# Kernel tuning notes

Measured on AMD Instinct MI355X. Metric: run time of the kernel, lower is better.

The kernel has to match this reference:

```python
import jax, jax.numpy as jnp
import numpy as np

NUM_HEADS = 8
NUM_LAYERS = 6
NUM_POINTS = 25
# TrajParamIndex: X=0,Y=1,Z=2,VX=3,VY=4,AX=5,AY=6,YAW=7,LENGTH=8,WIDTH=9,HEIGHT=10


def _unit_cube_points(n=NUM_POINTS):
    m = int(np.sqrt(n))
    lin = np.linspace(-1.0, 1.0, m)
    pts = []
    for dim in range(3):
        for sign in (-1.0, 1.0):
            a, b = np.meshgrid(lin, lin, indexing='ij')
            s = np.full_like(a, sign)
            if dim == 0:
                p = np.stack([s, a, b], -1)
            elif dim == 1:
                p = np.stack([a, s, b], -1)
            else:
                p = np.stack([a, b, s], -1)
            pts.append(p.reshape(-1, 3))
    return jnp.asarray(np.concatenate(pts, 0), jnp.float32)  # [150,3]


def _ln(x, g, b):
    m = x.mean(-1, keepdims=True)
    v = ((x - m) ** 2).mean(-1, keepdims=True)
    return (x - m) / jnp.sqrt(v + 1e-5) * g + b


def _mha(q, k, v, wi, bi, wo, bo):
    E = q.shape[-1]
    d = E // NUM_HEADS
    qq = q @ wi[:E].T + bi[:E]
    kk = k @ wi[E:2 * E].T + bi[E:2 * E]
    vv = v @ wi[2 * E:].T + bi[2 * E:]
    B, S, _ = qq.shape
    Sk = kk.shape[1]
    qh = qq.reshape(B, S, NUM_HEADS, d)
    kh = kk.reshape(B, Sk, NUM_HEADS, d)
    vh = vv.reshape(B, Sk, NUM_HEADS, d)
    att = jnp.einsum('bqhd,bkhd->bhqk', qh, kh) / jnp.sqrt(jnp.float32(d))
    att = jax.nn.softmax(att, axis=-1)
    o = jnp.einsum('bhqk,bkhd->bqhd', att, vh).reshape(B, S, E)
    return o @ wo.T + bo


def _bilinear(feat, uv, valid):
    # feat [B,C,H,W], uv [B,M,2] in [0,1] (u along W), valid [B,M] -> [B,M,C]
    B, C, H, W = feat.shape
    px = uv[..., 0] * (W - 1)
    py = uv[..., 1] * (H - 1)
    x0 = jnp.floor(px)
    y0 = jnp.floor(py)
    wx = px - x0
    wy = py - y0
    x0i = jnp.clip(x0, 0, W - 1).astype(jnp.int32)
    x1i = jnp.clip(x0 + 1, 0, W - 1).astype(jnp.int32)
    y0i = jnp.clip(y0, 0, H - 1).astype(jnp.int32)
    y1i = jnp.clip(y0 + 1, 0, H - 1).astype(jnp.int32)
    flat = feat.reshape(B, C, H * W)
    take = jax.vmap(lambda f, i: f[:, i])  # [C,HW],[M] -> [C,M]
    f00 = take(flat, y0i * W + x0i)
    f01 = take(flat, y0i * W + x1i)
    f10 = take(flat, y1i * W + x0i)
    f11 = take(flat, y1i * W + x1i)
    wxb = wx[:, None, :]
    wyb = wy[:, None, :]
    out = (f00 * (1 - wxb) * (1 - wyb) + f01 * wxb * (1 - wyb)
           + f10 * (1 - wxb) * wyb + f11 * wxb * wyb)
    out = out * valid[:, None, :].astype(out.dtype)
    return out.transpose(0, 2, 1)


def _transform_points(box_pts, tp, ego_t, dt):
    # box_pts [B,N,P,3] local, tp [B,N,11], ego_t [B,4] (x,y,yaw,ts), dt [B]
    yaw = tp[..., 7][..., None]  # [B,N,1]
    c, s = jnp.cos(yaw), jnp.sin(yaw)
    lx, ly, lz = box_pts[..., 0], box_pts[..., 1], box_pts[..., 2]
    rx = lx * c - ly * s
    ry = lx * s + ly * c
    dtb = dt[:, None]  # [B,1]
    cx = tp[..., 0] + tp[..., 3] * dtb + 0.5 * tp[..., 5] * dtb ** 2  # [B,N]
    cy = tp[..., 1] + tp[..., 4] * dtb + 0.5 * tp[..., 6] * dtb ** 2
    cz = tp[..., 2]
    wx = rx + cx[..., None]
    wy = ry + cy[..., None]
    wz = lz + cz[..., None]
    ex = ego_t[:, 0][:, None, None]
    ey = ego_t[:, 1][:, None, None]
    eyaw = ego_t[:, 2][:, None, None]
    pxr = wx - ex
    pyr = wy - ey
    gx = pxr * jnp.cos(eyaw) + pyr * jnp.sin(eyaw)
    gy = -pxr * jnp.sin(eyaw) + pyr * jnp.cos(eyaw)
    return jnp.stack([gx, gy, wz], -1)


def _project(wp, cal):
    # wp [B,N,P,3], cal [B,8] = fx,fy,cx,cy,tx,ty,tz,cam_yaw -> uv in [0,1], valid
    fx, fy, cx0, cy0, tx, ty, tz, cyaw = [cal[:, i][:, None, None] for i in range(8)]
    px = wp[..., 0] - tx
    py = wp[..., 1] - ty
    pz = wp[..., 2] - tz
    fwd = px * jnp.cos(cyaw) + py * jnp.sin(cyaw)
    left = -px * jnp.sin(cyaw) + py * jnp.cos(cyaw)
    zc = fwd
    xc = -left
    yc = -pz
    vz = zc > 0.1
    zs = jnp.maximum(zc, 0.1)
    u = fx * xc / zs + cx0
    v = fy * yc / zs + cy0
    valid = vz & (u >= 0) & (u < 1) & (v >= 0) & (v < 1)
    return jnp.stack([u, v], -1), valid


def _forward(features, calib, ego_states, queries, query_pos,
             traj_w1, traj_b1, traj_w2, traj_b2,
             fm_w1, fm_b1, fm_w2, fm_b2,
             sa_in_w, sa_in_b, sa_out_w, sa_out_b,
             ca_in_w, ca_in_b, ca_out_w, ca_out_b,
             l1_w, l1_b, l2_w, l2_b,
             n1_g, n1_b, n2_g, n2_b, n3_g, n3_b):
    unit = _unit_cube_points()  # [P,3]
    P = unit.shape[0]
    cams, B, T = features.shape[0], features.shape[1], features.shape[2]
    Cf = features.shape[3]
    N = queries.shape[0]

    def traj_head(x):
        return jax.nn.relu(x @ traj_w1.T + traj_b1) @ traj_w2.T + traj_b2

    def feature_mlp(x):
        return jax.nn.relu(x @ fm_w1.T + fm_b1) @ fm_w2.T + fm_b2

    q = jnp.broadcast_to(queries[None], (B, N, queries.shape[1]))
    outputs = []
    for li in range(NUM_LAYERS):
        tp = traj_head(q)  # [B,N,11]
        outputs.append(tp)
        dims = tp[..., 8:11][:, :, None, :]  # [B,N,1,3] (L,W,H)
        box_pts = unit[None, None] * dims  # [B,N,P,3]
        acc = jnp.zeros((B, N, Cf), jnp.float32)
        for t in range(T):
            dt = ego_states[:, t, 3] - ego_states[:, -1, 3]  # [B]
            wp = _transform_points(box_pts, tp, ego_states[:, t], dt)
            for ci in range(cams):
                uv, valid = _project(wp, calib[ci])
                samp = _bilinear(features[ci, :, t], uv.reshape(B, N * P, 2),
                                 valid.reshape(B, N * P))  # [B,N*P,Cf]
                acc = acc + samp.reshape(B, N, P, Cf).sum(axis=2)
        agg = acc / jnp.float32(P * T * cams)
        mem = feature_mlp(agg)  # [B,N,Cf]
        # refine layer li (called without query_pos in decoder forward)
        sa = _mha(q, q, q, sa_in_w[li], sa_in_b[li], sa_out_w[li], sa_out_b[li])
        q = _ln(q + sa, n1_g[li], n1_b[li])
        ca = _mha(q, mem, mem, ca_in_w[li], ca_in_b[li], ca_out_w[li], ca_out_b[li])
        q = _ln(q + ca, n2_g[li], n2_b[li])
        ff = jax.nn.relu(q @ l1_w[li].T + l1_b[li]) @ l2_w[li].T + l2_b[li]
        q = _ln(q + ff, n3_g[li], n3_b[li])
    outputs.append(traj_head(q))
    return jnp.stack(outputs)  # [L+1,B,N,11]


def setup_inputs() -> dict:
    key = jax.random.key(0)
    ks = jax.random.split(key, 32)
    cams, B, T, Cf, H, W = 6, 1, 2, 256, 64, 160
    N, E, Dff, L = 128, 256, 512, NUM_LAYERS

    def rn(k, shape, scale=0.05):
        return jax.random.normal(k, shape, jnp.float32) * scale

    features = jax.random.normal(ks[0], (cams, B, T, Cf, H, W), jnp.float32)
    # calibration: fx,fy,cx,cy,tx,ty,tz,cam_yaw; cameras 8m behind origin along view dir
    cal = np.zeros((cams, B, 8), np.float32)
    for ci in range(cams):
        cyaw = ci * (2 * np.pi / cams)
        cal[ci, :, 0] = 1.2
        cal[ci, :, 1] = 1.6
        cal[ci, :, 2] = 0.5
        cal[ci, :, 3] = 0.5
        cal[ci, :, 4] = -8.0 * np.cos(cyaw)
        cal[ci, :, 5] = -8.0 * np.sin(cyaw)
        cal[ci, :, 6] = -0.5
        cal[ci, :, 7] = cyaw
    calib = jnp.asarray(cal)
    ego = np.zeros((B, T, 4), np.float32)
    for t in range(T):
        ego[:, t, 0] = 0.5 * t
        ego[:, t, 2] = 0.01 * t
        ego[:, t, 3] = 0.1 * t
    ego_states = jnp.asarray(ego)
    return {
        'features': features, 'calib': calib, 'ego_states': ego_states,
        'queries': rn(ks[1], (N, E), 1.0), 'query_pos': rn(ks[2], (N, E), 1.0),
        'traj_w1': rn(ks[3], (Dff, E)), 'traj_b1': jnp.zeros((Dff,), jnp.float32),
        'traj_w2': rn(ks[4], (11, Dff)), 'traj_b2': jnp.zeros((11,), jnp.float32),
        'fm_w1': rn(ks[5], (Dff, E)), 'fm_b1': jnp.zeros((Dff,), jnp.float32),
        'fm_w2': rn(ks[6], (E, Dff)), 'fm_b2': jnp.zeros((E,), jnp.float32),
        'sa_in_w': rn(ks[7], (L, 3 * E, E)), 'sa_in_b': jnp.zeros((L, 3 * E), jnp.float32),
        'sa_out_w': rn(ks[8], (L, E, E)), 'sa_out_b': jnp.zeros((L, E), jnp.float32),
        'ca_in_w': rn(ks[9], (L, 3 * E, E)), 'ca_in_b': jnp.zeros((L, 3 * E), jnp.float32),
        'ca_out_w': rn(ks[10], (L, E, E)), 'ca_out_b': jnp.zeros((L, E), jnp.float32),
        'l1_w': rn(ks[11], (L, Dff, E)), 'l1_b': jnp.zeros((L, Dff), jnp.float32),
        'l2_w': rn(ks[12], (L, E, Dff)), 'l2_b': jnp.zeros((L, E), jnp.float32),
        'n1_g': jnp.ones((L, E), jnp.float32), 'n1_b': jnp.zeros((L, E), jnp.float32),
        'n2_g': jnp.ones((L, E), jnp.float32), 'n2_b': jnp.zeros((L, E), jnp.float32),
        'n3_g': jnp.ones((L, E), jnp.float32), 'n3_b': jnp.zeros((L, E), jnp.float32),
    }


def reference(features, calib, ego_states, queries, query_pos,
              traj_w1, traj_b1, traj_w2, traj_b2,
              fm_w1, fm_b1, fm_w2, fm_b2,
              sa_in_w, sa_in_b, sa_out_w, sa_out_b,
              ca_in_w, ca_in_b, ca_out_w, ca_out_b,
              l1_w, l1_b, l2_w, l2_b,
              n1_g, n1_b, n2_g, n2_b, n3_g, n3_b):
    return _forward(features, calib, ego_states, queries, query_pos,
                    traj_w1, traj_b1, traj_w2, traj_b2,
                    fm_w1, fm_b1, fm_w2, fm_b2,
                    sa_in_w, sa_in_b, sa_out_w, sa_out_b,
                    ca_in_w, ca_in_b, ca_out_w, ca_out_b,
                    l1_w, l1_b, l2_w, l2_b,
                    n1_g, n1_b, n2_g, n2_b, n3_g, n3_b)
```

## Files before the change

### kernel.cpp

```cpp
#include <hip/hip_runtime.h>
#include <stdint.h>

typedef unsigned short u16;

#define DEV static __device__ __forceinline__

DEV float b2f(u16 u){ return __uint_as_float(((uint32_t)u) << 16); }
DEV u16 f2b(float f){ uint32_t x = __float_as_uint(f); return (u16)((x + 0x7fffu + ((x >> 16) & 1u)) >> 16); }
DEV int imin(int a, int b){ return a < b ? a : b; }
DEV int imax(int a, int b){ return a > b ? a : b; }

DEV int is_f32(const void* cal){
  float a = ((const float*)cal)[0];
  return (fabsf(a - 1.2f) < 1e-2f) ? 1 : 0;
}

DEV float ld(const void* p, size_t i, int f32){
  return f32 ? ((const float*)p)[i] : b2f(((const u16*)p)[i]);
}

__device__ float4 g_sawT[6*256*768/4];
__device__ float4 g_sowT[6*256*256/4];
__device__ float4 g_cawT[6*256*768/4];
__device__ float4 g_cowT[6*256*256/4];
__device__ float4 g_l1wT[6*256*512/4];
__device__ float4 g_l2wT[6*512*256/4];
__device__ float4 g_tw1T[256*512/4];
__device__ float4 g_fw1T[256*512/4];
__device__ float4 g_fw2T[512*256/4];

DEV float dotP(const float* x, const float4* wP, int col, const int N, const int K){
  const float4* p = wP + col;
  const float4* x4 = (const float4*)x;
  float s0=0.f,s1=0.f,s2=0.f,s3=0.f;
  #pragma unroll 8
  for(int k4 = 0; k4 < K/4; k4++){
    float4 w = p[(size_t)k4*N];
    float4 xv = x4[k4];
    s0 += xv.x*w.x; s1 += xv.y*w.y; s2 += xv.z*w.z; s3 += xv.w*w.w;
  }
  return (s0+s1)+(s2+s3);
}

DEV void dot2P(const float* x, const float4* wP, int c0, int c1, const int N,
               float* r0, float* r1){
  const float4* p0 = wP + c0;
  const float4* p1 = wP + c1;
  const float4* x4 = (const float4*)x;
  float a0=0,a1=0,a2=0,a3=0,b0=0,b1=0,b2=0,b3=0;
  #pragma unroll 8
  for(int k4 = 0; k4 < 64; k4++){
    float4 xv = x4[k4];
    float4 w0 = p0[(size_t)k4*N];
    float4 w1 = p1[(size_t)k4*N];
    a0+=xv.x*w0.x; a1+=xv.y*w0.y; a2+=xv.z*w0.z; a3+=xv.w*w0.w;
    b0+=xv.x*w1.x; b1+=xv.y*w1.y; b2+=xv.z*w1.z; b3+=xv.w*w1.w;
  }
  *r0=(a0+a1)+(a2+a3); *r1=(b0+b1)+(b2+b3);
}

DEV void dot3P(const float* x, const float4* wP, int t, float* r0, float* r1, float* r2){
  const float4* p0 = wP + t;
  const float4* p1 = wP + t + 256;
  const float4* p2 = wP + t + 512;
  const float4* x4 = (const float4*)x;
  float a0=0,a1=0,a2=0,a3=0,b0=0,b1=0,b2=0,b3=0,c0=0,c1=0,c2=0,c3=0;
  #pragma unroll 4
  for(int k4 = 0; k4 < 64; k4++){
    float4 xv = x4[k4];
    float4 w0 = p0[(size_t)k4*768];
    float4 w1 = p1[(size_t)k4*768];
    float4 w2 = p2[(size_t)k4*768];
    a0+=xv.x*w0.x; a1+=xv.y*w0.y; a2+=xv.z*w0.z; a3+=xv.w*w0.w;
    b0+=xv.x*w1.x; b1+=xv.y*w1.y; b2+=xv.z*w1.z; b3+=xv.w*w1.w;
    c0+=xv.x*w2.x; c1+=xv.y*w2.y; c2+=xv.z*w2.z; c3+=xv.w*w2.w;
  }
  *r0=(a0+a1)+(a2+a3); *r1=(b0+b1)+(b2+b3); *r2=(c0+c1)+(c2+c3);
}

DEV void kv_store_k(float* kT, int t, int qi, float val){
  int hh = t >> 5, i = t & 31;
  kT[((size_t)(hh*1024 + (i>>2)*128 + qi))*4 + (i&3)] = val;
}
DEV void kv_store_v(float* vP, int t, int qi, float val){
  vP[((size_t)((qi>>2)*256 + t))*4 + (qi&3)] = val;
}

DEV float attn_score(const float* qv, const float* kT, int hh, int k){
  const float4* kp = (const float4*)kT + hh*1024 + k;
  const float4* xq = (const float4*)(qv + hh*32);
  float s0=0.f, s1=0.f;
  #pragma unroll
  for(int i4 = 0; i4 < 8; i4 += 2){
    float4 w0 = kp[i4*128], w1 = kp[(i4+1)*128];
    float4 x0 = xq[i4],     x1 = xq[i4+1];
    s0 += x0.x*w0.x + x0.y*w0.y + x0.z*w0.z + x0.w*w0.w;
    s1 += x1.x*w1.x + x1.y*w1.y + x1.z*w1.z + x1.w*w1.w;
  }
  return s0+s1;
}

DEV float attn_av(const float* s, const float* vP, int hh, int t){
  const float4* vp = (const float4*)vP + t;
  const float4* sp = (const float4*)(s + hh*128);
  float a0=0.f, a1=0.f;
  #pragma unroll 8
  for(int k4 = 0; k4 < 32; k4 += 2){
    float4 w0 = vp[(size_t)k4*256], w1 = vp[(size_t)(k4+1)*256];
    float4 s0 = sp[k4],             s1 = sp[k4+1];
    a0 += s0.x*w0.x + s0.y*w0.y + s0.z*w0.z + s0.w*w0.w;
    a1 += s1.x*w1.x + s1.y*w1.y + s1.z*w1.z + s1.w*w1.w;
  }
  return a0+a1;
}

DEV float bsum256(float v, float* buf){
  int t = threadIdx.x;
  for(int off = 32; off > 0; off >>= 1) v += __shfl_xor(v, off);
  if((t & 63) == 0) buf[t >> 6] = v;
  __syncthreads();
  float r = buf[0] + buf[1] + buf[2] + buf[3];
  __syncthreads();
  return r;
}

DEV float lnorm(float r, const void* g, const void* b, size_t off, float* buf, int f32){
  float m = bsum256(r, buf) * (1.f/256.f);
  float d = r - m;
  float v = bsum256(d*d, buf) * (1.f/256.f);
  return d * rsqrtf(v + 1e-5f) * ld(g, off + threadIdx.x, f32) + ld(b, off + threadIdx.x, f32);
}

DEV void traj_headT(const float* qn, const void* b1, const void* w2, const void* b2,
                    float* hbuf, float* tp, void* out, int slot, int qi, int f32){
  int t = threadIdx.x;
  float h0, h1;
  dot2P(qn, g_tw1T, t, t + 256, 512, &h0, &h1);
  hbuf[t]     = fmaxf(0.f, ld(b1, t, f32)     + h0);
  hbuf[t+256] = fmaxf(0.f, ld(b1, t+256, f32) + h1);
  __syncthreads();
  if(t < 176){
    int o = t >> 4, lane = t & 15;
    float s = 0.f;
    for(int k = lane; k < 512; k += 16) s += hbuf[k] * ld(w2, o*512 + k, f32);
    for(int off = 8; off > 0; off >>= 1) s += __shfl_down(s, off, 16);
    if(lane == 0){
      s += ld(b2, o, f32);
      tp[qi*11 + o] = s;
      int oi = (slot*128 + qi)*11 + o;
      if(f32) ((float*)out)[oi] = s; else ((u16*)out)[oi] = f2b(s);
    }
  }
  __syncthreads();
}

DEV void softmax8(float* s){
  int t = threadIdx.x;
  int hh = t >> 5, lane = t & 31;
  float m = -1e30f;
  for(int k = lane; k < 128; k += 32) m = fmaxf(m, s[hh*128 + k]);
  for(int off = 16; off > 0; off >>= 1) m = fmaxf(m, __shfl_xor(m, off, 32));
  float ss = 0.f;
  for(int k = lane; k < 128; k += 32){
    float e = __expf(s[hh*128 + k] - m);
    s[hh*128 + k] = e; ss += e;
  }
  for(int off = 16; off > 0; off >>= 1) ss += __shfl_xor(ss, off, 32);
  float inv = 1.f / ss;
  for(int k = lane; k < 128; k += 32) s[hh*128 + k] *= inv;
}

__global__ __launch_bounds__(256) void k_wt(
    const void* saw, const void* sow, const void* caw, const void* cow,
    const void* l1w, const void* l2w, const void* tw1, const void* fw1, const void* fw2,
    const void* cal){
  int f32 = is_f32(cal);
  int t = threadIdx.x;
  __shared__ __align__(16) float tile[64*65];
  int bid = blockIdx.x;
  const void* src; float* dst; int N, K, NB, KB;
  if(bid < 288)      { src = saw; dst = (float*)g_sawT; N=768; K=256; NB=12; KB=4; }
  else if(bid < 384) { src = sow; dst = (float*)g_sowT; N=256; K=256; NB=4;  KB=4; bid -= 288; }
  else if(bid < 672) { src = caw; dst = (float*)g_cawT; N=768; K=256; NB=12; KB=4; bid -= 384; }
  else if(bid < 768) { src = cow; dst = (float*)g_cowT; N=256; K=256; NB=4;  KB=4; bid -= 672; }
  else if(bid < 960) { src = l1w; dst = (float*)g_l1wT; N=512; K=256; NB=8;  KB=4; bid -= 768; }
  else if(bid < 1152){ src = l2w; dst = (float*)g_l2wT; N=256; K=512; NB=4;  KB=8; bid -= 960; }
  else if(bid < 1184){ src = tw1; dst = (float*)g_tw1T; N=512; K=256; NB=8;  KB=4; bid -= 1152; }
  else if(bid < 1216){ src = fw1; dst = (float*)g_fw1T; N=512; K=256; NB=8;  KB=4; bid -= 1184; }
  else               { src = fw2; dst = (float*)g_fw2T; N=256; K=512; NB=4;  KB=8; bid -= 1216; }
  int nb = bid % NB;
  int kb = (bid / NB) % KB;
  int l  = bid / (NB*KB);
  for(int it = 0; it < 16; it++){
    int n = it*4 + (t >> 6);
    int k = t & 63;
    tile[n*65 + k] = ld(src, ((size_t)l*N + nb*64 + n)*K + kb*64 + k, f32);
  }
  __syncthreads();
  int kl = t & 3, nn = (t >> 2) & 15, wv = t >> 6;
  int n_local = wv*16 + nn;
  for(int k4 = 0; k4 < 16; k4++){
    int kcol = k4*4 + kl;
    size_t addr = (size_t)l*K*N + (((size_t)(kb*16 + k4))*N + nb*64 + n_local)*4 + kl;
    dst[addr] = tile[n_local*65 + kcol];
  }
}

__global__ __launch_bounds__(256) void k_trinit(const void* feat, u16* FTb, int use_ft,
    const void* queries, const void* tb1, const void* tw2, const void* tb2,
    const void* sab, const void* cal,
    float* q, float* tp, float* qrow, float* kTsa, float* vsa, float* acc, void* out){
  int f32 = is_f32(cal);
  int t = threadIdx.x;
  __shared__ __align__(16) uint32_t smem[64*65];
  if(blockIdx.x < 128){
    float* qn   = (float*)smem;
    float* hbuf = (float*)smem + 256;
    int qi = blockIdx.x;
    float v = ld(queries, qi*256 + t, f32);
    qn[t] = v; q[qi*256 + t] = v;
    __syncthreads();
    traj_headT(qn, tb1, tw2, tb2, hbuf, tp, out, 0, qi, f32);
    float c0, c1, c2;
    dot3P(qn, g_sawT, t, &c0, &c1, &c2);
    qrow[qi*256 + t] = ld(sab, t, f32)       + c0;
    kv_store_k(kTsa, t, qi, ld(sab, t + 256, f32) + c1);
    kv_store_v(vsa,  t, qi, ld(sab, t + 512, f32) + c2);
    acc[qi*256 + t] = 0.f;
    return;
  }
  if(!use_ft) return;
  int orig = blockIdx.x - 128;
  int swz  = (orig & 7) * 960 + (orig >> 3);
  int pch = swz % 160; int g = swz / 160;
  int cc = g & 3; int e = g >> 2;
  size_t rowbase = (size_t)(e*256 + cc*64);
  size_t poff = (size_t)pch*64;
  if(f32){
    #pragma unroll
    for(int pass = 0; pass < 4; pass++){
      int ch = pass*16 + (t >> 4);
      int pos = (t & 15)*4;
      const float* sp = (const float*)feat + (rowbase + ch)*10240 + poff + pos;
      float4 v = *(const float4*)sp;
      smem[(pos+0)*65 + ch] = f2b(v.x);
      smem[(pos+1)*65 + ch] = f2b(v.y);
      smem[(pos+2)*65 + ch] = f2b(v.z);
      smem[(pos+3)*65 + ch] = f2b(v.w);
    }
  } else {
    #pragma unroll
    for(int pass = 0; pass < 4; pass++){
      int ch = pass*16 + (t >> 4);
      int pos = (t & 15)*4;
      const u16* sp = (const u16*)feat + (rowbase + ch)*10240 + poff + pos;
      ushort4 v = *(const ushort4*)sp;
      smem[(pos+0)*65 + ch] = v.x;
      smem[(pos+1)*65 + ch] = v.y;
      smem[(pos+2)*65 + ch] = v.z;
      smem[(pos+3)*65 + ch] = v.w;
    }
  }
  __syncthreads();
  #pragma unroll
  for(int pass = 0; pass < 4; pass++){
    int pos = pass*16 + (t >> 4);
    int ch = (t & 15)*4;
    ushort4 v;
    v.x = (u16)smem[pos*65 + ch];
    v.y = (u16)smem[pos*65 + ch+1];
    v.z = (u16)smem[pos*65 + ch+2];
    v.w = (u16)smem[pos*65 + ch+3];
    *(ushort4*)&FTb[((size_t)(e*10240) + poff + pos)*256 + cc*64 + ch] = v;
  }
}

__global__ __launch_bounds__(256, 2) void k_samsa(const u16* FTb, const void* feat, int use_ft,
    const void* cal, const void* ego, const float* tp, float* acc,
    const float* q, const float* qrow, const float* kTsa, const float* vsa,
    const void* sob, const void* n1g, const void* n1b, const void* cab,
    int li, float* qs, float* qq){
  int t = threadIdx.x;
  int f32 = is_f32(cal);
  __shared__ __align__(16) float xa[256];
  __shared__ __align__(16) float s[1024];
  __shared__ __align__(16) float h[512];
  __shared__ float buf[8];
  __shared__ float tps[11];
  __shared__ int4  soff[152];
  __shared__ float4 sw[152];
  __shared__ float spx[152], spy[152];
  __shared__ int sval[152];
  __shared__ int plist[152];
  __shared__ int pcnt;

  if(blockIdx.x < 128){
    int qi = blockIdx.x;
    xa[t] = qrow[qi*256 + t];
    __syncthreads();
    for(int rep = 0; rep < 4; rep++){
      int idx = t + rep*256; int hh = idx >> 7, k = idx & 127;
      s[idx] = attn_score(xa, kTsa, hh, k) * 0.1767766952966369f;
    }
    __syncthreads();
    softmax8(s);
    __syncthreads();
    h[t] = attn_av(s, vsa, t >> 5, t);
    __syncthreads();
    float pr = ld(sob, (size_t)li*256 + t, f32) + dotP(h, g_sowT + (size_t)li*16384, t, 256, 256);
    float r = q[qi*256 + t] + pr;
    float y = lnorm(r, n1g, n1b, (size_t)li*256, buf, f32);
    qs[qi*256 + t] = y;
    __syncthreads();
    xa[t] = y;
    __syncthreads();
    qq[qi*256 + t] = ld(cab, (size_t)li*768 + t, f32)
                   + dotP(xa, g_cawT + (size_t)li*49152, t, 768, 256);
    return;
  }

  int sb = blockIdx.x - 128;
  int ob = (sb & 7) * 192 + (sb >> 3);
  int qi = ob & 127, e = ob >> 7;
  int ci = e >> 1, tt = e & 1;
  if(t == 0) pcnt = 0;
  if(t < 11) tps[t] = tp[qi*11 + t];
  __syncthreads();
  if(t < 150){
    float dt = ld(ego, tt*4 + 3, f32) - ld(ego, 7, f32);
    int face = t/25, rr = t%25, ii = rr/5, jj = rr%5;
    float av = -1.f + 0.5f*ii, bv = -1.f + 0.5f*jj;
    float sg = (face & 1) ? 1.f : -1.f; int dim = face >> 1;
    float ux = (dim == 0) ? sg : av;
    float uy = (dim == 0) ? av : ((dim == 1) ? sg : bv);
    float uz = (dim == 2) ? sg : bv;
    float lx = ux*tps[8], ly = uy*tps[9], lz = uz*tps[10];
    float yaw = tps[7];
    float cyw = cosf(yaw), syw = sinf(yaw);
    float rx = lx*cyw - ly*syw, ry = lx*syw + ly*cyw;
    float dt2 = 0.5f*dt*dt;
    float cxx = tps[0] + tps[3]*dt + tps[5]*dt2;
    float cyy = tps[1] + tps[4]*dt + tps[6]*dt2;
    float wx = rx + cxx, wy = ry + cyy, wz = lz + tps[2];
    float ex = ld(ego, tt*4, f32), ey = ld(ego, tt*4 + 1, f32), eyaw = ld(ego, tt*4 + 2, f32);
    float ce = cosf(eyaw), se = sinf(eyaw);
    float pxr = wx - ex, pyr = wy - ey;
    float gx = pxr*ce + pyr*se, gy = -pxr*se + pyr*ce;
    float fx = ld(cal, ci*8, f32),   fy = ld(cal, ci*8+1, f32);
    float cx0 = ld(cal, ci*8+2, f32), cy0 = ld(cal, ci*8+3, f32);
    float tx = ld(cal, ci*8+4, f32), ty = ld(cal, ci*8+5, f32);
    float tz = ld(cal, ci*8+6, f32), cw = ld(cal, ci*8+7, f32);
    float cc = cosf(cw), sc = sinf(cw);
    float pxc = gx - tx, pyc = gy - ty, pzc = wz - tz;
    float zc = pxc*cc + pyc*sc;
    float left = -pxc*sc + pyc*cc;
    float xc = -left, yc = -pzc;
    float zs = fmaxf(zc, 0.1f);
    float u = fx*xc/zs + cx0, vv = fy*yc/zs + cy0;
    bool val = (zc > 0.1f) && (u >= 0.f) && (u < 1.f) && (vv >= 0.f) && (vv < 1.f);
    float px = u*159.f, py = vv*63.f;
    spx[t] = px; spy[t] = py;
    float x0f = floorf(px), y0f = floorf(py);
    float wxf = px - x0f, wyf = py - y0f;
    int x0 = imin(imax((int)x0f, 0), 159), y0 = imin(imax((int)y0f, 0), 63);
    int x1 = imin(x0 + 1, 159), y1 = imin(y0 + 1, 63);
    soff[t] = make_int4((y0*160 + x0)*256, (y0*160 + x1)*256,
                        (y1*160 + x0)*256, (y1*160 + x1)*256);
    sw[t] = make_float4((1.f-wxf)*(1.f-wyf), wxf*(1.f-wyf), (1.f-wxf)*wyf, wxf*wyf);
    sval[t] = val ? 1 : 0;
    if(val){ int ix = atomicAdd(&pcnt, 1); plist[ix] = t; }
  }
  __syncthreads();
  float a = 0.f;
  if(use_ft){
    const u16* base = FTb + (size_t)e*10240*256 + t;
    int np = pcnt;
    int pp = 0;
    for(; pp + 4 <= np; pp += 4){
      int p0 = plist[pp], p1 = plist[pp+1], p2 = plist[pp+2], p3 = plist[pp+3];
      int4 o0 = soff[p0]; int4 o1 = soff[p1]; int4 o2 = soff[p2]; int4 o3 = soff[p3];
      float4 w0 = sw[p0]; float4 w1 = sw[p1]; float4 w2 = sw[p2]; float4 w3 = sw[p3];
      float v00 = b2f(base[o0.x]), v01 = b2f(base[o0.y]), v02 = b2f(base[o0.z]), v03 = b2f(base[o0.w]);
      float v10 = b2f(base[o1.x]), v11 = b2f(base[o1.y]), v12 = b2f(base[o1.z]), v13 = b2f(base[o1.w]);
      float v20 = b2f(base[o2.x]), v21 = b2f(base[o2.y]), v22 = b2f(base[o2.z]), v23 = b2f(base[o2.w]);
      float v30 = b2f(base[o3.x]), v31 = b2f(base[o3.y]), v32 = b2f(base[o3.z]), v33 = b2f(base[o3.w]);
      a += w0.x*v00 + w0.y*v01 + w0.z*v02 + w0.w*v03;
      a += w1.x*v10 + w1.y*v11 + w1.z*v12 + w1.w*v13;
      a += w2.x*v20 + w2.y*v21 + w2.z*v22 + w2.w*v23;
      a += w3.x*v30 + w3.y*v31 + w3.z*v32 + w3.w*v33;
    }
    for(; pp < np; pp++){
      int p = plist[pp];
      int4 o = soff[p]; float4 w = sw[p];
      a += w.x*b2f(base[o.x]) + w.y*b2f(base[o.y])
         + w.z*b2f(base[o.z]) + w.w*b2f(base[o.w]);
    }
  } else {
    size_t pc = ((size_t)e*256 + t)*10240;
    for(int p = 0; p < 150; p++){
      if(!sval[p]) continue;
      float px = spx[p], py = spy[p];
      float x0f = floorf(px), y0f = floorf(py);
      float wxf = px - x0f, wyf = py - y0f;
      int x0 = imin(imax((int)x0f, 0), 159), y0 = imin(imax((int)y0f, 0), 63);
      int x1 = imin(x0 + 1, 159), y1 = imin(y0 + 1, 63);
      float w00 = (1.f-wxf)*(1.f-wyf), w01 = wxf*(1.f-wyf), w10 = (1.f-wxf)*wyf, w11 = wxf*wyf;
      a += w00*ld(feat, pc + y0*160 + x0, f32) + w01*ld(feat, pc + y0*160 + x1, f32)
         + w10*ld(feat, pc + y1*160 + x0, f32) + w11*ld(feat, pc + y1*160 + x1, f32);
    }
  }
  atomicAdd(&acc[qi*256 + t], a);
}

__global__ __launch_bounds__(256, 2) void k_mk(const float* acc,
    const void* fb1, const void* fb2, const void* cab, const void* cal,
    int li, float* kvK, float* kvV){
  __shared__ __align__(16) float xa[256];
  __shared__ __align__(16) float h[512];
  int t = threadIdx.x, qi = blockIdx.x;
  int f32 = is_f32(cal);
  xa[t] = acc[qi*256 + t] * (1.f/1800.f);
  __syncthreads();
  float h0, h1;
  dot2P(xa, g_fw1T, t, t + 256, 512, &h0, &h1);
  h[t]     = fmaxf(0.f, ld(fb1, t, f32)     + h0);
  h[t+256] = fmaxf(0.f, ld(fb1, t+256, f32) + h1);
  __syncthreads();
  float m = ld(fb2, t, f32) + dotP(h, g_fw2T, t, 256, 512);
  __syncthreads();
  xa[t] = m;
  __syncthreads();
  const float4* cawT = g_cawT + (size_t)li*49152;
  float kk, vv;
  dot2P(xa, cawT, 256 + t, 512 + t, 768, &kk, &vv);
  size_t bo = (size_t)li*768;
  kv_store_k(kvK, t, qi, ld(cab, bo + 256 + t, f32) + kk);
  kv_store_v(kvV, t, qi, ld(cab, bo + 512 + t, f32) + vv);
}

__global__ __launch_bounds__(256, 2) void k_ca(const float* qs, const float* qq,
    const float* kvK, const float* kvV,
    const void* cob, const void* n2g, const void* n2b,
    const void* l1b, const void* l2b, const void* n3g, const void* n3b,
    const void* tb1, const void* tw2, const void* tb2, const void* sab, const void* cal,
    int li, int have_next,
    float* qout, float* qrow, float* kTsa, float* vsa,
    float* tp, float* acc, void* out){
  __shared__ __align__(16) float qv[256]; __shared__ __align__(16) float s[1024];
  __shared__ __align__(16) float o[256];  __shared__ __align__(16) float q2[256];
  __shared__ __align__(16) float h[512];  __shared__ float buf[8];
  int t = threadIdx.x, qi = blockIdx.x;
  int f32 = is_f32(cal);
  qv[t] = qq[qi*256 + t];
  __syncthreads();
  for(int rep = 0; rep < 4; rep++){
    int idx = t + rep*256; int hh = idx >> 7, k = idx & 127;
    s[idx] = attn_score(qv, kvK, hh, k) * 0.1767766952966369f;
  }
  __syncthreads();
  softmax8(s);
  __syncthreads();
  o[t] = attn_av(s, kvV, t >> 5, t);
  __syncthreads();
  float pr = ld(cob, (size_t)li*256 + t, f32) + dotP(o, g_cowT + (size_t)li*16384, t, 256, 256);
  float r = qs[qi*256 + t] + pr;
  float y = lnorm(r, n2g, n2b, (size_t)li*256, buf, f32);
  q2[t] = y;
  __syncthreads();
  float h0, h1;
  dot2P(q2, g_l1wT + (size_t)li*32768, t, t + 256, 512, &h0, &h1);
  h[t]     = fmaxf(0.f, ld(l1b, (size_t)li*512 + t, f32)     + h0);
  h[t+256] = fmaxf(0.f, ld(l1b, (size_t)li*512 + t+256, f32) + h1);
  __syncthreads();
  float ff = ld(l2b, (size_t)li*256 + t, f32) + dotP(h, g_l2wT + (size_t)li*32768, t, 256, 512);
  float r3 = q2[t] + ff;
  float y3 = lnorm(r3, n3g, n3b, (size_t)li*256, buf, f32);
  qout[qi*256 + t] = y3;
  __syncthreads();
  q2[t] = y3;
  __syncthreads();
  traj_headT(q2, tb1, tw2, tb2, h, tp, out, li + 1, qi, f32);
  if(have_next){
    float c0, c1, c2;
    dot3P(q2, g_sawT + (size_t)(li+1)*49152, t, &c0, &c1, &c2);
    size_t sb = (size_t)(li+1)*768;
    qrow[qi*256 + t] = ld(sab, sb + t, f32) + c0;
    kv_store_k(kTsa, t, qi, ld(sab, sb + 256 + t, f32) + c1);
    kv_store_v(vsa,  t, qi, ld(sab, sb + 512 + t, f32) + c2);
  }
  acc[qi*256 + t] = 0.f;
}

extern "C" void kernel_launch(void* const* d_in, const int* in_sizes, int n_in,
                              void* d_out, int out_size, void* d_ws, size_t ws_size,
                              hipStream_t stream){
  const void* feat    = d_in[0];
  const void* calib   = d_in[1];
  const void* ego     = d_in[2];
  const void* queries = d_in[3];
  const void* tw1 = d_in[5];  const void* tb1 = d_in[6];
  const void* tw2 = d_in[7];  const void* tb2 = d_in[8];
  const void* fw1 = d_in[9];  const void* fb1 = d_in[10];
  const void* fw2 = d_in[11]; const void* fb2 = d_in[12];
  const void* saw = d_in[13]; const void* sab = d_in[14];
  const void* sow = d_in[15]; const void* sob = d_in[16];
  const void* caw = d_in[17]; const void* cab = d_in[18];
  const void* cow = d_in[19]; const void* cob = d_in[20];
  const void* l1w = d_in[21]; const void* l1b = d_in[22];
  const void* l2w = d_in[23]; const void* l2b = d_in[24];
  const void* n1g = d_in[25]; const void* n1b = d_in[26];
  const void* n2g = d_in[27]; const void* n2b = d_in[28];
  const void* n3g = d_in[29]; const void* n3b = d_in[30];

  float* ws   = (float*)d_ws;
  float* q    = ws + 16;
  float* qs   = ws + 32784;
  float* tp   = ws + 65552;
  float* qrow = ws + 67088;
  float* kTsa = ws + 99856;
  float* vsa  = ws + 132624;
  float* kvK  = ws + 165392;
  float* kvV  = ws + 198160;
  float* qq   = ws + 230928;
  float* acc  = ws + 263696;
  u16*   FTb  = (u16*)(ws + 296464);
  size_t need = (size_t)296464*4 + (size_t)12*10240*256*2;
  int use_ft = (ws_size >= need) ? 1 : 0;

  k_wt<<<1248, 256, 0, stream>>>(saw, sow, caw, cow, l1w, l2w, tw1, fw1, fw2, calib);
  k_trinit<<<7808, 256, 0, stream>>>(feat, FTb, use_ft,
                                     queries, tb1, tw2, tb2, sab, calib,
                                     q, tp, qrow, kTsa, vsa, acc, d_out);
  for(int li = 0; li < 6; li++){
    k_samsa<<<1664, 256, 0, stream>>>(FTb, feat, use_ft, calib, ego, tp, acc,
                                      q, qrow, kTsa, vsa, sob, n1g, n1b, cab,
                                      li, qs, qq);
    k_mk<<<128, 256, 0, stream>>>(acc, fb1, fb2, cab, calib, li, kvK, kvV);
    int hn = (li < 5) ? 1 : 0;
    k_ca<<<128, 256, 0, stream>>>(qs, qq, kvK, kvV, cob, n2g, n2b,
                                  l1b, l2b, n3g, n3b,
                                  tb1, tw2, tb2, sab, calib, li, hn,
                                  q, qrow, kTsa, vsa, tp, acc, d_out);
  }
  (void)in_sizes; (void)n_in; (void)out_size;
}
```

Baseline: 1.027 ms.

## Gather bf16 feature pairs with 32-bit loads and split sample points across half-blocks

The bilinear gather in k_samsa now has each thread load a 32-bit word holding two adjacent bf16 channels. The block's two halves each handle half of the valid sample points, and the partial sums are reduced through shared memory before the atomic add. This halves the number of load instructions per channel and gives more independent work per thread, at the cost of an extra sync and shared-memory reduction. The transpose kernel that builds the bf16 channel-last buffer is also simplified to scalar loads with a 2-wide store, dropping the earlier vectorized global reads and block swizzle.

```diff
diff --git a/kernel.cpp b/kernel.cpp
--- a/kernel.cpp
+++ b/kernel.cpp
@@ -212,10 +212,10 @@
     float* q, float* tp, float* qrow, float* kTsa, float* vsa, float* acc, void* out){
   int f32 = is_f32(cal);
   int t = threadIdx.x;
-  __shared__ __align__(16) uint32_t smem[64*65];
+  __shared__ __align__(16) float smem[64*65];
   if(blockIdx.x < 128){
-    float* qn   = (float*)smem;
-    float* hbuf = (float*)smem + 256;
+    float* qn   = smem;
+    float* hbuf = smem + 256;
     int qi = blockIdx.x;
     float v = ld(queries, qi*256 + t, f32);
     qn[t] = v; q[qi*256 + t] = v;
@@ -230,48 +230,21 @@
     return;
   }
   if(!use_ft) return;
-  int orig = blockIdx.x - 128;
-  int swz  = (orig & 7) * 960 + (orig >> 3);
-  int pch = swz % 160; int g = swz / 160;
-  int cc = g & 3; int e = g >> 2;
-  size_t rowbase = (size_t)(e*256 + cc*64);
-  size_t poff = (size_t)pch*64;
-  if(f32){
-    #pragma unroll
-    for(int pass = 0; pass < 4; pass++){
-      int ch = pass*16 + (t >> 4);
-      int pos = (t & 15)*4;
-      const float* sp = (const float*)feat + (rowbase + ch)*10240 + poff + pos;
-      float4 v = *(const float4*)sp;
-      smem[(pos+0)*65 + ch] = f2b(v.x);
-      smem[(pos+1)*65 + ch] = f2b(v.y);
-      smem[(pos+2)*65 + ch] = f2b(v.z);
-      smem[(pos+3)*65 + ch] = f2b(v.w);
-    }
-  } else {
-    #pragma unroll
-    for(int pass = 0; pass < 4; pass++){
-      int ch = pass*16 + (t >> 4);
-      int pos = (t & 15)*4;
-      const u16* sp = (const u16*)feat + (rowbase + ch)*10240 + poff + pos;
-      ushort4 v = *(const ushort4*)sp;
-      smem[(pos+0)*65 + ch] = v.x;
-      smem[(pos+1)*65 + ch] = v.y;
-      smem[(pos+2)*65 + ch] = v.z;
-      smem[(pos+3)*65 + ch] = v.w;
-    }
-  }
-  __syncthreads();
-  #pragma unroll
-  for(int pass = 0; pass < 4; pass++){
-    int pos = pass*16 + (t >> 4);
-    int ch = (t & 15)*4;
-    ushort4 v;
-    v.x = (u16)smem[pos*65 + ch];
-    v.y = (u16)smem[pos*65 + ch+1];
-    v.z = (u16)smem[pos*65 + ch+2];
-    v.w = (u16)smem[pos*65 + ch+3];
-    *(ushort4*)&FTb[((size_t)(e*10240) + poff + pos)*256 + cc*64 + ch] = v;
+  int bid = blockIdx.x - 128;
+  int cc = bid & 3; int rest = bid >> 2;
+  int pch = rest % 160; int e = rest / 160;
+  for(int it = 0; it < 16; it++){
+    int c = it*4 + (t >> 6);
+    int p = t & 63;
+    smem[p*65 + c] = ld(feat, ((size_t)(e*256 + cc*64 + c))*10240 + pch*64 + p, f32);
+  }
+  __syncthreads();
+  for(int it = 0; it < 8; it++){
+    int p = it*8 + (t >> 5);
+    int c = (t & 31)*2;
+    ushort2 v;
+    v.x = f2b(smem[p*65 + c]); v.y = f2b(smem[p*65 + c + 1]);
+    *(ushort2*)&FTb[((size_t)(e*10240 + pch*64 + p))*256 + cc*64 + c] = v;
   }
 }
 
@@ -364,38 +337,53 @@
     float wxf = px - x0f, wyf = py - y0f;
     int x0 = imin(imax((int)x0f, 0), 159), y0 = imin(imax((int)y0f, 0), 63);
     int x1 = imin(x0 + 1, 159), y1 = imin(y0 + 1, 63);
-    soff[t] = make_int4((y0*160 + x0)*256, (y0*160 + x1)*256,
-                        (y1*160 + x0)*256, (y1*160 + x1)*256);
+    soff[t] = make_int4((y0*160 + x0)*128, (y0*160 + x1)*128,
+                        (y1*160 + x0)*128, (y1*160 + x1)*128);
     sw[t] = make_float4((1.f-wxf)*(1.f-wyf), wxf*(1.f-wyf), (1.f-wxf)*wyf, wxf*wyf);
     sval[t] = val ? 1 : 0;
     if(val){ int ix = atomicAdd(&pcnt, 1); plist[ix] = t; }
   }
   __syncthreads();
-  float a = 0.f;
   if(use_ft){
-    const u16* base = FTb + (size_t)e*10240*256 + t;
+    int c2 = (t & 127) * 2;
+    int half = t >> 7;
+    const uint32_t* base = (const uint32_t*)FTb + (size_t)e*10240*128 + (c2 >> 1);
     int np = pcnt;
-    int pp = 0;
-    for(; pp + 4 <= np; pp += 4){
-      int p0 = plist[pp], p1 = plist[pp+1], p2 = plist[pp+2], p3 = plist[pp+3];
-      int4 o0 = soff[p0]; int4 o1 = soff[p1]; int4 o2 = soff[p2]; int4 o3 = soff[p3];
-      float4 w0 = sw[p0]; float4 w1 = sw[p1]; float4 w2 = sw[p2]; float4 w3 = sw[p3];
-      float v00 = b2f(base[o0.x]), v01 = b2f(base[o0.y]), v02 = b2f(base[o0.z]), v03 = b2f(base[o0.w]);
-      float v10 = b2f(base[o1.x]), v11 = b2f(base[o1.y]), v12 = b2f(base[o1.z]), v13 = b2f(base[o1.w]);
-      float v20 = b2f(base[o2.x]), v21 = b2f(base[o2.y]), v22 = b2f(base[o2.z]), v23 = b2f(base[o2.w]);
-      float v30 = b2f(base[o3.x]), v31 = b2f(base[o3.y]), v32 = b2f(base[o3.z]), v33 = b2f(base[o3.w]);
-      a += w0.x*v00 + w0.y*v01 + w0.z*v02 + w0.w*v03;
-      a += w1.x*v10 + w1.y*v11 + w1.z*v12 + w1.w*v13;
-      a += w2.x*v20 + w2.y*v21 + w2.z*v22 + w2.w*v23;
-      a += w3.x*v30 + w3.y*v31 + w3.z*v32 + w3.w*v33;
+    int split = (np + 1) >> 1;
+    int lo = half ? split : 0;
+    int hi = half ? np : split;
+    float a0 = 0.f, a1 = 0.f;
+    int pp = lo;
+    for(; pp + 2 <= hi; pp += 2){
+      int p0 = plist[pp], p1 = plist[pp+1];
+      int4 o0 = soff[p0]; int4 o1 = soff[p1];
+      float4 w0 = sw[p0]; float4 w1 = sw[p1];
+      uint32_t u00 = base[o0.x], u01 = base[o0.y], u02 = base[o0.z], u03 = base[o0.w];
+      uint32_t u10 = base[o1.x], u11 = base[o1.y], u12 = base[o1.z], u13 = base[o1.w];
+      a0 += w0.x*__uint_as_float(u00<<16) + w0.y*__uint_as_float(u01<<16)
+          + w0.z*__uint_as_float(u02<<16) + w0.w*__uint_as_float(u03<<16);
+      a1 += w0.x*__uint_as_float(u00&0xffff0000u) + w0.y*__uint_as_float(u01&0xffff0000u)
+          + w0.z*__uint_as_float(u02&0xffff0000u) + w0.w*__uint_as_float(u03&0xffff0000u);
+      a0 += w1.x*__uint_as_float(u10<<16) + w1.y*__uint_as_float(u11<<16)
+          + w1.z*__uint_as_float(u12<<16) + w1.w*__uint_as_float(u13<<16);
+      a1 += w1.x*__uint_as_float(u10&0xffff0000u) + w1.y*__uint_as_float(u11&0xffff0000u)
+          + w1.z*__uint_as_float(u12&0xffff0000u) + w1.w*__uint_as_float(u13&0xffff0000u);
     }
-    for(; pp < np; pp++){
+    for(; pp < hi; pp++){
       int p = plist[pp];
       int4 o = soff[p]; float4 w = sw[p];
-      a += w.x*b2f(base[o.x]) + w.y*b2f(base[o.y])
-         + w.z*b2f(base[o.z]) + w.w*b2f(base[o.w]);
+      uint32_t u0 = base[o.x], u1 = base[o.y], u2 = base[o.z], u3 = base[o.w];
+      a0 += w.x*__uint_as_float(u0<<16) + w.y*__uint_as_float(u1<<16)
+          + w.z*__uint_as_float(u2<<16) + w.w*__uint_as_float(u3<<16);
+      a1 += w.x*__uint_as_float(u0&0xffff0000u) + w.y*__uint_as_float(u1&0xffff0000u)
+          + w.z*__uint_as_float(u2&0xffff0000u) + w.w*__uint_as_float(u3&0xffff0000u);
     }
+    s[half*256 + c2]     = a0;
+    s[half*256 + c2 + 1] = a1;
+    __syncthreads();
+    atomicAdd(&acc[qi*256 + t], s[t] + s[256 + t]);
   } else {
+    float a = 0.f;
     size_t pc = ((size_t)e*256 + t)*10240;
     for(int p = 0; p < 150; p++){
       if(!sval[p]) continue;
@@ -408,8 +396,8 @@
       a += w00*ld(feat, pc + y0*160 + x0, f32) + w01*ld(feat, pc + y0*160 + x1, f32)
          + w10*ld(feat, pc + y1*160 + x0, f32) + w11*ld(feat, pc + y1*160 + x1, f32);
     }
-  }
-  atomicAdd(&acc[qi*256 + t], a);
+    atomicAdd(&acc[qi*256 + t], a);
+  }
 }
 
 __global__ __launch_bounds__(256, 2) void k_mk(const float* acc,
```

Result: faster. 970.2 us (-5.5%).
